# Performance work log

Hardware: AMD Instinct MI355X
Metric: run time of the kernel (lower is better)

The kernel has to match this reference:

```python
import jax, jax.numpy as jnp
import numpy as np

SEQ = 8192
IN_DIM = 1024
HIDDEN_DIM = 2048
N_EXPERTS = 8
TOPK = 2


def setup_inputs() -> dict:
    key = jax.random.key(0)
    ks = jax.random.split(key, 6)
    scale = 0.02
    inp = jax.random.normal(ks[0], (SEQ, IN_DIM), jnp.float32)
    weights = jax.random.uniform(ks[1], (SEQ, TOPK), jnp.float32)
    selections = jax.random.randint(ks[2], (SEQ, TOPK), 0, N_EXPERTS, jnp.int32)
    up_proj = jax.random.normal(ks[3], (HIDDEN_DIM * N_EXPERTS, IN_DIM), jnp.float32) * scale
    gate_proj = jax.random.normal(ks[4], (HIDDEN_DIM * N_EXPERTS, IN_DIM), jnp.float32) * scale
    down_proj = jax.random.normal(ks[5], (HIDDEN_DIM * N_EXPERTS, IN_DIM), jnp.float32) * scale
    return {"inp": inp, "weights": weights, "up_proj": up_proj,
            "gate_proj": gate_proj, "down_proj": down_proj, "selections": selections}


def reference(inp, weights, up_proj, gate_proj, down_proj, selections):
    seq, in_dim = inp.shape
    topk = selections.shape[-1]
    # dispatch: replicate each token topk times -> (seq*topk, in_dim)
    x = jnp.broadcast_to(inp[:, None, :], (seq, topk, in_dim)).reshape(-1, in_dim)
    e_ids = selections.reshape(-1)  # (seq*topk,) expert id per dispatched token
    W_up = up_proj.reshape(N_EXPERTS, HIDDEN_DIM, in_dim)
    W_gate = gate_proj.reshape(N_EXPERTS, HIDDEN_DIM, in_dim)
    W_down = down_proj.reshape(N_EXPERTS, HIDDEN_DIM, in_dim)
    out = jnp.zeros_like(x)
    # grouped (block-sparse) GEMM: loop over the small fixed expert set,
    # masking tokens not routed to this expert (gelu(0)*0 = 0, so math matches).
    for e in range(N_EXPERTS):
        mask = (e_ids == e)[:, None]
        xe = jnp.where(mask, x, 0.0)
        h = xe @ W_up[e].T        # (seq*topk, hidden)
        g = xe @ W_gate[e].T      # (seq*topk, hidden)
        out = out + jnp.where(mask, (jax.nn.gelu(g) * h) @ W_down[e], 0.0)
    # combine: weighted sum over topk expert outputs per token
    return (out.reshape(seq, topk, in_dim) * weights[:, :, None]).sum(axis=1)
```

## Files before the change

kernel.cpp:

```cpp
#include <hip/hip_runtime.h>


#define SEQ 8192
#define IN_DIM 1024
#define HID 2048
#define NEXP 8
#define TOPK 2
#define NSLOT (SEQ * TOPK)

#define BM 128
#define BK 64
#define BM1 256
#define MAX_T1 72

typedef unsigned short ushort_t;
typedef __bf16 bf16x8 __attribute__((ext_vector_type(8)));
typedef float f32x4 __attribute__((ext_vector_type(4)));

__device__ __forceinline__ ushort_t f2bf(float f) {
    union { float f; unsigned u; } v;
    v.f = f;
    unsigned r = v.u + 0x7FFFu + ((v.u >> 16) & 1u);
    return (ushort_t)(r >> 16);
}

__device__ __forceinline__ float gelu_tanh(float x) {
    float u = 0.7978845608028654f * x * (1.0f + 0.044715f * x * x);
    return x / (1.0f + __expf(-2.0f * u));
}

__device__ __forceinline__ void async16(const void* g, void* l) {
    __builtin_amdgcn_global_load_lds(
        (const __attribute__((address_space(1))) unsigned int*)g,
        (__attribute__((address_space(3))) unsigned int*)l, 16, 0, 0);
}

__global__ void cast_bf16_kernel(const float* __restrict__ in,
                                 ushort_t* __restrict__ out, int n) {
    int i = (blockIdx.x * blockDim.x + threadIdx.x) * 4;
    if (i >= n) return;
    float4 v = *(const float4*)(in + i);
    union { ushort_t u[4]; uint2 v; } o;
    o.u[0] = f2bf(v.x); o.u[1] = f2bf(v.y);
    o.u[2] = f2bf(v.z); o.u[3] = f2bf(v.w);
    *(uint2*)(out + i) = o.v;
}

__global__ void transpose_cast_kernel(const float* __restrict__ in,
                                      ushort_t* __restrict__ out) {
    __shared__ float tile[32][33];
    int e = blockIdx.z;
    int d0 = blockIdx.x * 32, h0 = blockIdx.y * 32;
    int tx = threadIdx.x & 31, ty = threadIdx.x >> 5;
    const float* src = in + (size_t)e * HID * IN_DIM;
    for (int j = 0; j < 32; j += 8)
        tile[ty + j][tx] = src[(size_t)(h0 + ty + j) * IN_DIM + d0 + tx];
    __syncthreads();
    ushort_t* dst = out + (size_t)e * IN_DIM * HID;
    for (int j = 0; j < 32; j += 8)
        dst[(size_t)(d0 + ty + j) * HID + h0 + tx] = f2bf(tile[tx][ty + j]);
}

__global__ void route_kernel(const int* __restrict__ sel,
                             const float* __restrict__ wts,
                             int* __restrict__ meta,
                             int* __restrict__ stok,
                             int* __restrict__ sinv) {
    __shared__ int lc[256][NEXP];
    __shared__ int tot[NEXP];
    __shared__ int s_off[NEXP + 1];
    int t = threadIdx.x;
    int cnt[NEXP];
#pragma unroll
    for (int e = 0; e < NEXP; e++) cnt[e] = 0;
    int base = t * (NSLOT / 256);
    for (int i = 0; i < NSLOT / 256; i++) cnt[sel[base + i]]++;
#pragma unroll
    for (int e = 0; e < NEXP; e++) lc[t][e] = cnt[e];
    __syncthreads();
    if (t < NEXP) {
        int run = 0;
        for (int i = 0; i < 256; i++) { int v = lc[i][t]; lc[i][t] = run; run += v; }
        tot[t] = run;
    }
    __syncthreads();
    if (t == 0) {
        int o = 0;
        for (int e = 0; e < NEXP; e++) { s_off[e] = o; o += tot[e]; }
        s_off[NEXP] = o;
        for (int e = 0; e <= NEXP; e++) meta[e] = s_off[e];
        int nt = 0;
        for (int e = 0; e < NEXP; e++) {
            int c = s_off[e + 1] - s_off[e];
            int m = (c + BM - 1) / BM;
            for (int i = 0; i < m; i++) { meta[32 + 2 * nt] = e; meta[33 + 2 * nt] = i; nt++; }
        }
        meta[16] = nt;
    }
    __syncthreads();
    int cur[NEXP];
#pragma unroll
    for (int e = 0; e < NEXP; e++) cur[e] = s_off[e] + lc[t][e];
    for (int i = 0; i < NSLOT / 256; i++) {
        int slot = base + i;
        int e = sel[slot];
        int pos = cur[e]++;
        stok[pos] = slot >> 1;
        sinv[slot] = pos;
    }
}

#define ST_A(b, h, koff) {                                                 \
        async16(pA[h][0] + (koff), &AT[b][h][(w * 16) * BK]);              \
        async16(pA[h][1] + (koff), &AT[b][h][(w * 16 + 8) * BK]); }
#define ST_U(b, koff) {                                                    \
        async16(pU[0] + (koff), &UT[b][(w * 16) * BK]);                    \
        async16(pU[1] + (koff), &UT[b][(w * 16 + 8) * BK]); }
#define ST_G(b, koff) {                                                    \
        async16(pG[0] + (koff), &GT[b][(w * 16) * BK]);                    \
        async16(pG[1] + (koff), &GT[b][(w * 16 + 8) * BK]); }

#define RD_A(b, mb) {                                                      \
        _Pragma("unroll") for (int mi = 0; mi < 4; mi++)                   \
        _Pragma("unroll") for (int kh = 0; kh < 2; kh++)                   \
            a[mi][kh] = *(const bf16x8*)&AT[b][wm][                        \
                ((mb) + mi * 16 + r4) * BK + (((kh * 4 + q) ^ sw7) << 3)]; }
#define RD_U(b) {                                                          \
        _Pragma("unroll") for (int ni = 0; ni < 2; ni++)                   \
        _Pragma("unroll") for (int kh = 0; kh < 2; kh++)                   \
            bu[ni][kh] = *(const bf16x8*)&UT[b][                           \
                (wn * 32 + ni * 16 + r4) * BK + (((kh * 4 + q) ^ sw7) << 3)]; }
#define RD_G(b) {                                                          \
        _Pragma("unroll") for (int ni = 0; ni < 2; ni++)                   \
        _Pragma("unroll") for (int kh = 0; kh < 2; kh++)                   \
            bg[ni][kh] = *(const bf16x8*)&GT[b][                           \
                (wn * 32 + ni * 16 + r4) * BK + (((kh * 4 + q) ^ sw7) << 3)]; }

#define MM(ACC, mb2, BB) {                                                 \
        _Pragma("unroll") for (int mi = 0; mi < 4; mi++)                   \
        _Pragma("unroll") for (int ni = 0; ni < 2; ni++)                   \
        _Pragma("unroll") for (int kh = 0; kh < 2; kh++)                   \
            ACC[(mb2) + mi][ni] = __builtin_amdgcn_mfma_f32_16x16x32_bf16( \
                a[mi][kh], BB[ni][kh], ACC[(mb2) + mi][ni], 0, 0, 0); }

#define BARRIER __builtin_amdgcn_s_barrier()
#define LGKM0 asm volatile("s_waitcnt lgkmcnt(0)" ::: "memory")
#define VMW2 asm volatile("s_waitcnt vmcnt(2)" ::: "memory")
#define VMW0 asm volatile("s_waitcnt vmcnt(0)" ::: "memory")
#define PRIO1 __builtin_amdgcn_s_setprio(1)
#define PRIO0 __builtin_amdgcn_s_setprio(0)

#define KPRO                                                               \
    ST_A(0, 0, 0); ST_A(0, 1, 0); ST_U(0, 0); ST_G(0, 0);                  \
    ST_A(1, 0, 64);                                                        \
    VMW2; BARRIER;

#define KBODY_FULL                                                         \
    RD_A(0, 0); RD_U(0); ST_A(1, 1, 64); BARRIER; LGKM0;                   \
    PRIO1; MM(accH, 0, bu); PRIO0; BARRIER;                                \
    RD_G(0); ST_U(1, 64); BARRIER; LGKM0;                                  \
    PRIO1; MM(accG, 0, bg); PRIO0; BARRIER;                                \
    RD_A(0, 64); ST_G(1, 64); BARRIER; LGKM0;                              \
    PRIO1; MM(accG, 4, bg); PRIO0; BARRIER;                                \
    ST_A(0, 0, 128); VMW2; BARRIER;                                        \
    PRIO1; MM(accH, 4, bu); PRIO0; BARRIER;                                \
    RD_A(1, 0); RD_U(1); ST_A(0, 1, 128); BARRIER; LGKM0;                  \
    PRIO1; MM(accH, 0, bu); PRIO0; BARRIER;                                \
    RD_G(1); ST_U(0, 128); BARRIER; LGKM0;                                 \
    PRIO1; MM(accG, 0, bg); PRIO0; BARRIER;                                \
    RD_A(1, 64); ST_G(0, 128); BARRIER; LGKM0;                             \
    PRIO1; MM(accG, 4, bg); PRIO0; BARRIER;                                \
    ST_A(1, 0, 192); VMW2; BARRIER;                                        \
    PRIO1; MM(accH, 4, bu); PRIO0; BARRIER;

#define KBODY_ADV {                                                        \
    pA[0][0] += 128; pA[0][1] += 128; pA[1][0] += 128; pA[1][1] += 128;    \
    pU[0] += 128; pU[1] += 128; pG[0] += 128; pG[1] += 128; }

#define KBODY_TAIL                                                         \
    RD_A(0, 0); RD_U(0); ST_A(1, 1, 64); BARRIER; LGKM0;                   \
    PRIO1; MM(accH, 0, bu); PRIO0; BARRIER;                                \
    RD_G(0); ST_U(1, 64); BARRIER; LGKM0;                                  \
    PRIO1; MM(accG, 0, bg); PRIO0; BARRIER;                                \
    RD_A(0, 64); ST_G(1, 64); BARRIER; LGKM0;                              \
    PRIO1; MM(accG, 4, bg); PRIO0; BARRIER;                                \
    VMW0; BARRIER;                                                         \
    PRIO1; MM(accH, 4, bu); PRIO0; BARRIER;                                \
    RD_A(1, 0); RD_U(1); BARRIER; LGKM0;                                   \
    PRIO1; MM(accH, 0, bu); PRIO0; BARRIER;                                \
    RD_G(1); BARRIER; LGKM0;                                               \
    PRIO1; MM(accG, 0, bg); PRIO0; BARRIER;                                \
    RD_A(1, 64); BARRIER; LGKM0;                                           \
    PRIO1; MM(accG, 4, bg); PRIO0; BARRIER;                                \
    PRIO1; MM(accH, 4, bu); PRIO0;

#define TILE_DERIVE(tile)                                                  \
    int e = -1, mt = 0, accT = 0;                                          \
    _Pragma("unroll")                                                      \
    for (int ee = 0; ee < NEXP; ee++) {                                    \
        int c = meta[ee + 1] - meta[ee];                                   \
        int m = (c + BM1 - 1) >> 8;                                        \
        if ((tile) >= accT && (tile) < accT + m) { e = ee; mt = (tile) - accT; } \
        accT += m;                                                         \
    }                                                                      \
    if (e < 0) return;                                                     \
    int off = meta[e];                                                     \
    int cnt = meta[e + 1] - off;                                           \
    int m0 = mt * BM1;

__global__ __launch_bounds__(512, 2) void gemm1_kernel(
    const ushort_t* __restrict__ X,
    const ushort_t* __restrict__ U,
    const ushort_t* __restrict__ G,
    const int* __restrict__ meta,
    const int* __restrict__ stok,
    ushort_t* __restrict__ act) {
    __shared__ __align__(16) ushort_t AT[2][2][128 * BK];
    __shared__ __align__(16) ushort_t UT[2][128 * BK];
    __shared__ __align__(16) ushort_t GT[2][128 * BK];
    __shared__ int s_tok[BM1];

    int id = blockIdx.x + MAX_T1 * blockIdx.y;
    int wi = (id & 7) * 144 + (id >> 3);
    int tile = wi % MAX_T1;
    int n0 = (wi / MAX_T1) * 128;

    TILE_DERIVE(tile);

    int tid = threadIdx.x;
    if (tid < BM1) {
        int r = m0 + tid;
        if (r >= cnt) r = cnt - 1;
        s_tok[tid] = stok[off + r];
    }
    __syncthreads();

    int lane = tid & 63;
    int w = tid >> 6;
    int wm = w >> 2;
    int wn = w & 3;
    int srow = lane >> 3;
    int schunk = lane & 7;
    int gchunk = schunk ^ srow;
    int r4 = lane & 15;
    int q = lane >> 4;
    int sw7 = r4 & 7;

    const ushort_t* pA[2][2];
#pragma unroll
    for (int h = 0; h < 2; h++)
#pragma unroll
        for (int j = 0; j < 2; j++) {
            int r = h * 128 + w * 16 + j * 8 + srow;
            pA[h][j] = X + (size_t)s_tok[r] * IN_DIM + gchunk * 8;
        }
    const ushort_t* Ue = U + ((size_t)e * HID + n0) * IN_DIM;
    const ushort_t* Ge = G + ((size_t)e * HID + n0) * IN_DIM;
    const ushort_t* pU[2];
    const ushort_t* pG[2];
#pragma unroll
    for (int j = 0; j < 2; j++) {
        int r = w * 16 + j * 8 + srow;
        pU[j] = Ue + (size_t)r * IN_DIM + gchunk * 8;
        pG[j] = Ge + (size_t)r * IN_DIM + gchunk * 8;
    }

    f32x4 accH[8][2], accG[8][2];
#pragma unroll
    for (int mi = 0; mi < 8; mi++)
#pragma unroll
        for (int ni = 0; ni < 2; ni++) {
            accH[mi][ni] = (f32x4){0.f, 0.f, 0.f, 0.f};
            accG[mi][ni] = (f32x4){0.f, 0.f, 0.f, 0.f};
        }

    bf16x8 a[4][2], bu[2][2], bg[2][2];

    KPRO;
#pragma unroll 1
    for (int i = 0; i < (IN_DIM / BK) / 2 - 1; ++i) {
        KBODY_FULL;
        KBODY_ADV;
    }
    KBODY_TAIL;

#pragma unroll
    for (int mf = 0; mf < 8; mf++) {
#pragma unroll
        for (int r = 0; r < 4; r++) {
            int row_local = wm * 128 + mf * 16 + q * 4 + r;
            int grow = m0 + row_local;
            if (grow >= cnt) continue;
            size_t orow = (size_t)(off + grow) * HID + n0 + wn * 32;
#pragma unroll
            for (int ni = 0; ni < 2; ni++) {
                float h = accH[mf][ni][r];
                float g = accG[mf][ni][r];
                act[orow + ni * 16 + r4] = f2bf(gelu_tanh(g) * h);
            }
        }
    }
}

__global__ __launch_bounds__(512, 2) void gemm2_kernel(
    const ushort_t* __restrict__ act,
    const ushort_t* __restrict__ DT,
    const int* __restrict__ meta,
    float* __restrict__ y) {
    __shared__ __align__(16) ushort_t AT[2][2][128 * BK];
    __shared__ __align__(16) ushort_t UT[2][128 * BK];
    __shared__ __align__(16) ushort_t GT[2][128 * BK];

    int id = blockIdx.x + MAX_T1 * blockIdx.y;
    int wi = (id & 7) * 36 + (id >> 3);
    int tile = wi % MAX_T1;
    int n0 = (wi / MAX_T1) * 256;

    TILE_DERIVE(tile);

    int tid = threadIdx.x;
    int lane = tid & 63;
    int w = tid >> 6;
    int wm = w >> 2;
    int wn = w & 3;
    int srow = lane >> 3;
    int schunk = lane & 7;
    int gchunk = schunk ^ srow;
    int r4 = lane & 15;
    int q = lane >> 4;
    int sw7 = r4 & 7;

    const ushort_t* Ae = act + (size_t)off * HID;
    const ushort_t* pA[2][2];
#pragma unroll
    for (int h = 0; h < 2; h++)
#pragma unroll
        for (int j = 0; j < 2; j++) {
            int ar = m0 + h * 128 + w * 16 + j * 8 + srow;
            if (ar >= cnt) ar = cnt - 1;
            pA[h][j] = Ae + (size_t)ar * HID + gchunk * 8;
        }
    const ushort_t* Be = DT + ((size_t)e * IN_DIM + n0) * HID;
    const ushort_t* pU[2];
    const ushort_t* pG[2];
#pragma unroll
    for (int j = 0; j < 2; j++) {
        int r = w * 16 + j * 8 + srow;
        pU[j] = Be + (size_t)r * HID + gchunk * 8;
        pG[j] = Be + (size_t)(128 + r) * HID + gchunk * 8;
    }

    f32x4 accH[8][2], accG[8][2];
#pragma unroll
    for (int mi = 0; mi < 8; mi++)
#pragma unroll
        for (int ni = 0; ni < 2; ni++) {
            accH[mi][ni] = (f32x4){0.f, 0.f, 0.f, 0.f};
            accG[mi][ni] = (f32x4){0.f, 0.f, 0.f, 0.f};
        }

    bf16x8 a[4][2], bu[2][2], bg[2][2];

    KPRO;
#pragma unroll 1
    for (int i = 0; i < (HID / BK) / 2 - 1; ++i) {
        KBODY_FULL;
        KBODY_ADV;
    }
    KBODY_TAIL;

#pragma unroll
    for (int mf = 0; mf < 8; mf++) {
#pragma unroll
        for (int r = 0; r < 4; r++) {
            int row_local = wm * 128 + mf * 16 + q * 4 + r;
            int grow = m0 + row_local;
            if (grow >= cnt) continue;
            float* orow = y + (size_t)(off + grow) * IN_DIM + n0 + wn * 32;
#pragma unroll
            for (int ni = 0; ni < 2; ni++) {
                orow[ni * 16 + r4] = accH[mf][ni][r];
                orow[128 + ni * 16 + r4] = accG[mf][ni][r];
            }
        }
    }
}

__global__ __launch_bounds__(256) void combine_kernel(
    const float* __restrict__ y,
    const float* __restrict__ wts,
    const int* __restrict__ sinv,
    float* __restrict__ out) {
    int tok = blockIdx.x;
    int c = threadIdx.x;
    int p0 = sinv[tok * 2], p1 = sinv[tok * 2 + 1];
    float w0 = wts[tok * 2], w1 = wts[tok * 2 + 1];
    float4 a = *(const float4*)(y + (size_t)p0 * IN_DIM + c * 4);
    float4 b = *(const float4*)(y + (size_t)p1 * IN_DIM + c * 4);
    float4 o;
    o.x = w0 * a.x + w1 * b.x;
    o.y = w0 * a.y + w1 * b.y;
    o.z = w0 * a.z + w1 * b.z;
    o.w = w0 * a.w + w1 * b.w;
    *(float4*)(out + (size_t)tok * IN_DIM + c * 4) = o;
}

extern "C" void kernel_launch(void* const* d_in, const int* in_sizes, int n_in,
                              void* d_out, int out_size, void* d_ws, size_t ws_size,
                              hipStream_t stream) {
    const float* inp  = (const float*)d_in[0];
    const float* wts  = (const float*)d_in[1];
    const float* up   = (const float*)d_in[2];
    const float* gate = (const float*)d_in[3];
    const float* down = (const float*)d_in[4];
    const int*   sel  = (const int*)d_in[5];
    float* out = (float*)d_out;

    char* ws = (char*)d_ws;
    ushort_t* inp_bf  = (ushort_t*)(ws);
    ushort_t* up_bf   = (ushort_t*)(ws + 16777216);
    ushort_t* gate_bf = (ushort_t*)(ws + 50331648);
    ushort_t* down_bf = (ushort_t*)(ws + 83886080);
    ushort_t* act     = (ushort_t*)(ws + 117440512);
    int*      stok    = (int*)(ws + 184549376);
    int*      sinv    = (int*)(ws + 184614912);
    int*      meta    = (int*)(ws + 184680448);
    float*    y       = (float*)(ws);

    cast_bf16_kernel<<<(SEQ * IN_DIM) / 1024, 256, 0, stream>>>(inp, inp_bf, SEQ * IN_DIM);
    cast_bf16_kernel<<<(NEXP * HID * IN_DIM) / 1024, 256, 0, stream>>>(up, up_bf, NEXP * HID * IN_DIM);
    cast_bf16_kernel<<<(NEXP * HID * IN_DIM) / 1024, 256, 0, stream>>>(gate, gate_bf, NEXP * HID * IN_DIM);
    transpose_cast_kernel<<<dim3(IN_DIM / 32, HID / 32, NEXP), 256, 0, stream>>>(down, down_bf);
    route_kernel<<<1, 256, 0, stream>>>(sel, wts, meta, stok, sinv);
    gemm1_kernel<<<dim3(MAX_T1, HID / 128), 512, 0, stream>>>(inp_bf, up_bf, gate_bf, meta, stok, act);
    gemm2_kernel<<<dim3(MAX_T1, IN_DIM / 256), 512, 0, stream>>>(act, down_bf, meta, y);
    combine_kernel<<<SEQ, 256, 0, stream>>>(y, wts, sinv, out);
}
```

Measured before the change: 567.1 us.

## Shrink gemm2 M-tile to 128 with new pipeline, fuse casts, remap XCD tiles

The down-projection GEMM now uses 128-row M tiles instead of 256, which roughly doubles the number of blocks (up to 140 tiles times 4 N-blocks) and reduces padding waste at the ragged end of each expert's token range. It gets a new double-buffered, single-k-step pipeline with finer vmcnt waits. The three input/up/gate fp32-to-bf16 cast launches are merged into one kernel. The gemm1 block-to-tile mapping is changed so that blocks on the same XCD share N-columns, aiming for better L2 reuse of weights. The trade-off is that smaller tiles lower per-block arithmetic intensity and reuse more weight traffic per output row.

```diff
diff --git a/kernel.cpp b/kernel.cpp
--- a/kernel.cpp
+++ b/kernel.cpp
@@ -12,6 +12,7 @@
 #define BK 64
 #define BM1 256
 #define MAX_T1 72
+#define MAX_T2 140
 
 typedef unsigned short ushort_t;
 typedef __bf16 bf16x8 __attribute__((ext_vector_type(8)));
@@ -35,15 +36,25 @@
         (__attribute__((address_space(3))) unsigned int*)l, 16, 0, 0);
 }
 
-__global__ void cast_bf16_kernel(const float* __restrict__ in,
-                                 ushort_t* __restrict__ out, int n) {
-    int i = (blockIdx.x * blockDim.x + threadIdx.x) * 4;
-    if (i >= n) return;
-    float4 v = *(const float4*)(in + i);
+__global__ void cast3_kernel(const float* __restrict__ inp,
+                             const float* __restrict__ up,
+                             const float* __restrict__ gate,
+                             ushort_t* __restrict__ o_inp,
+                             ushort_t* __restrict__ o_up,
+                             ushort_t* __restrict__ o_gate) {
+    const int N1 = SEQ * IN_DIM;
+    const int N2 = NEXP * HID * IN_DIM;
+    long i = (long)(blockIdx.x * blockDim.x + threadIdx.x) * 4;
+    const float* src;
+    ushort_t* dst;
+    if (i < N1)            { src = inp  + i;            dst = o_inp  + i; }
+    else if (i < N1 + N2)  { src = up   + (i - N1);     dst = o_up   + (i - N1); }
+    else                   { src = gate + (i - N1 - N2); dst = o_gate + (i - N1 - N2); }
+    float4 v = *(const float4*)src;
     union { ushort_t u[4]; uint2 v; } o;
     o.u[0] = f2bf(v.x); o.u[1] = f2bf(v.y);
     o.u[2] = f2bf(v.z); o.u[3] = f2bf(v.w);
-    *(uint2*)(out + i) = o.v;
+    *(uint2*)dst = o.v;
 }
 
 __global__ void transpose_cast_kernel(const float* __restrict__ in,
@@ -145,6 +156,7 @@
 
 #define BARRIER __builtin_amdgcn_s_barrier()
 #define LGKM0 asm volatile("s_waitcnt lgkmcnt(0)" ::: "memory")
+#define VMW4 asm volatile("s_waitcnt vmcnt(4)" ::: "memory")
 #define VMW2 asm volatile("s_waitcnt vmcnt(2)" ::: "memory")
 #define VMW0 asm volatile("s_waitcnt vmcnt(0)" ::: "memory")
 #define PRIO1 __builtin_amdgcn_s_setprio(1)
@@ -194,20 +206,6 @@
     PRIO1; MM(accG, 4, bg); PRIO0; BARRIER;                                \
     PRIO1; MM(accH, 4, bu); PRIO0;
 
-#define TILE_DERIVE(tile)                                                  \
-    int e = -1, mt = 0, accT = 0;                                          \
-    _Pragma("unroll")                                                      \
-    for (int ee = 0; ee < NEXP; ee++) {                                    \
-        int c = meta[ee + 1] - meta[ee];                                   \
-        int m = (c + BM1 - 1) >> 8;                                        \
-        if ((tile) >= accT && (tile) < accT + m) { e = ee; mt = (tile) - accT; } \
-        accT += m;                                                         \
-    }                                                                      \
-    if (e < 0) return;                                                     \
-    int off = meta[e];                                                     \
-    int cnt = meta[e + 1] - off;                                           \
-    int m0 = mt * BM1;
-
 __global__ __launch_bounds__(512, 2) void gemm1_kernel(
     const ushort_t* __restrict__ X,
     const ushort_t* __restrict__ U,
@@ -221,11 +219,23 @@
     __shared__ int s_tok[BM1];
 
     int id = blockIdx.x + MAX_T1 * blockIdx.y;
-    int wi = (id & 7) * 144 + (id >> 3);
-    int tile = wi % MAX_T1;
-    int n0 = (wi / MAX_T1) * 128;
-
-    TILE_DERIVE(tile);
+    int xcd = id & 7;
+    int j = id >> 3;
+    int tile = j >> 1;
+    int n0 = ((xcd << 1) | (j & 1)) * 128;
+
+    int e = -1, mt = 0, accT = 0;
+#pragma unroll
+    for (int ee = 0; ee < NEXP; ee++) {
+        int c = meta[ee + 1] - meta[ee];
+        int m = (c + BM1 - 1) >> 8;
+        if (tile >= accT && tile < accT + m) { e = ee; mt = tile - accT; }
+        accT += m;
+    }
+    if (e < 0) return;
+    int off = meta[e];
+    int cnt = meta[e + 1] - off;
+    int m0 = mt * BM1;
 
     int tid = threadIdx.x;
     if (tid < BM1) {
@@ -250,19 +260,19 @@
 #pragma unroll
     for (int h = 0; h < 2; h++)
 #pragma unroll
-        for (int j = 0; j < 2; j++) {
-            int r = h * 128 + w * 16 + j * 8 + srow;
-            pA[h][j] = X + (size_t)s_tok[r] * IN_DIM + gchunk * 8;
+        for (int jj = 0; jj < 2; jj++) {
+            int r = h * 128 + w * 16 + jj * 8 + srow;
+            pA[h][jj] = X + (size_t)s_tok[r] * IN_DIM + gchunk * 8;
         }
     const ushort_t* Ue = U + ((size_t)e * HID + n0) * IN_DIM;
     const ushort_t* Ge = G + ((size_t)e * HID + n0) * IN_DIM;
     const ushort_t* pU[2];
     const ushort_t* pG[2];
 #pragma unroll
-    for (int j = 0; j < 2; j++) {
-        int r = w * 16 + j * 8 + srow;
-        pU[j] = Ue + (size_t)r * IN_DIM + gchunk * 8;
-        pG[j] = Ge + (size_t)r * IN_DIM + gchunk * 8;
+    for (int jj = 0; jj < 2; jj++) {
+        int r = w * 16 + jj * 8 + srow;
+        pU[jj] = Ue + (size_t)r * IN_DIM + gchunk * 8;
+        pG[jj] = Ge + (size_t)r * IN_DIM + gchunk * 8;
     }
 
     f32x4 accH[8][2], accG[8][2];
@@ -307,16 +317,29 @@
     const ushort_t* __restrict__ DT,
     const int* __restrict__ meta,
     float* __restrict__ y) {
-    __shared__ __align__(16) ushort_t AT[2][2][128 * BK];
-    __shared__ __align__(16) ushort_t UT[2][128 * BK];
-    __shared__ __align__(16) ushort_t GT[2][128 * BK];
-
-    int id = blockIdx.x + MAX_T1 * blockIdx.y;
-    int wi = (id & 7) * 36 + (id >> 3);
-    int tile = wi % MAX_T1;
-    int n0 = (wi / MAX_T1) * 256;
-
-    TILE_DERIVE(tile);
+    __shared__ __align__(16) ushort_t AT2[2][128 * BK];
+    __shared__ __align__(16) ushort_t UT2[2][128 * BK];
+    __shared__ __align__(16) ushort_t GT2[2][128 * BK];
+
+    int id = blockIdx.x + MAX_T2 * blockIdx.y;
+    int xcd = id & 7;
+    int jj0 = id >> 3;
+    int wk = xcd * 70 + jj0;
+    int tile = wk >> 2;
+    int n0 = (wk & 3) * 256;
+
+    int e = -1, mt = 0, accT = 0;
+#pragma unroll
+    for (int ee = 0; ee < NEXP; ee++) {
+        int c = meta[ee + 1] - meta[ee];
+        int m = (c + 127) >> 7;
+        if (tile >= accT && tile < accT + m) { e = ee; mt = tile - accT; }
+        accT += m;
+    }
+    if (e < 0) return;
+    int off = meta[e];
+    int cnt = meta[e + 1] - off;
+    int m0 = mt * 128;
 
     int tid = threadIdx.x;
     int lane = tid & 63;
@@ -331,56 +354,98 @@
     int sw7 = r4 & 7;
 
     const ushort_t* Ae = act + (size_t)off * HID;
-    const ushort_t* pA[2][2];
-#pragma unroll
-    for (int h = 0; h < 2; h++)
-#pragma unroll
-        for (int j = 0; j < 2; j++) {
-            int ar = m0 + h * 128 + w * 16 + j * 8 + srow;
-            if (ar >= cnt) ar = cnt - 1;
-            pA[h][j] = Ae + (size_t)ar * HID + gchunk * 8;
+    const ushort_t* pA2[2];
+#pragma unroll
+    for (int jj = 0; jj < 2; jj++) {
+        int ar = m0 + w * 16 + jj * 8 + srow;
+        if (ar >= cnt) ar = cnt - 1;
+        pA2[jj] = Ae + (size_t)ar * HID + gchunk * 8;
+    }
+    const ushort_t* Be = DT + ((size_t)e * IN_DIM + n0) * HID;
+    const ushort_t* pU2[2];
+    const ushort_t* pG2[2];
+#pragma unroll
+    for (int jj = 0; jj < 2; jj++) {
+        int r = w * 16 + jj * 8 + srow;
+        pU2[jj] = Be + (size_t)r * HID + gchunk * 8;
+        pG2[jj] = Be + (size_t)(128 + r) * HID + gchunk * 8;
+    }
+
+    f32x4 accU[4][2], accGG[4][2];
+#pragma unroll
+    for (int mi = 0; mi < 4; mi++)
+#pragma unroll
+        for (int ni = 0; ni < 2; ni++) {
+            accU[mi][ni] = (f32x4){0.f, 0.f, 0.f, 0.f};
+            accGG[mi][ni] = (f32x4){0.f, 0.f, 0.f, 0.f};
         }
-    const ushort_t* Be = DT + ((size_t)e * IN_DIM + n0) * HID;
-    const ushort_t* pU[2];
-    const ushort_t* pG[2];
-#pragma unroll
-    for (int j = 0; j < 2; j++) {
-        int r = w * 16 + j * 8 + srow;
-        pU[j] = Be + (size_t)r * HID + gchunk * 8;
-        pG[j] = Be + (size_t)(128 + r) * HID + gchunk * 8;
-    }
-
-    f32x4 accH[8][2], accG[8][2];
-#pragma unroll
-    for (int mi = 0; mi < 8; mi++)
-#pragma unroll
-        for (int ni = 0; ni < 2; ni++) {
-            accH[mi][ni] = (f32x4){0.f, 0.f, 0.f, 0.f};
-            accG[mi][ni] = (f32x4){0.f, 0.f, 0.f, 0.f};
-        }
 
     bf16x8 a[4][2], bu[2][2], bg[2][2];
 
-    KPRO;
+#define ST_A2(b, koff) {                                                   \
+        async16(pA2[0] + (koff), &AT2[b][(w * 16) * BK]);                  \
+        async16(pA2[1] + (koff), &AT2[b][(w * 16 + 8) * BK]); }
+#define ST_U2(b, koff) {                                                   \
+        async16(pU2[0] + (koff), &UT2[b][(w * 16) * BK]);                  \
+        async16(pU2[1] + (koff), &UT2[b][(w * 16 + 8) * BK]); }
+#define ST_G2(b, koff) {                                                   \
+        async16(pG2[0] + (koff), &GT2[b][(w * 16) * BK]);                  \
+        async16(pG2[1] + (koff), &GT2[b][(w * 16 + 8) * BK]); }
+#define RD_A2(b) {                                                         \
+        _Pragma("unroll") for (int mi = 0; mi < 4; mi++)                   \
+        _Pragma("unroll") for (int kh = 0; kh < 2; kh++)                   \
+            a[mi][kh] = *(const bf16x8*)&AT2[b][                           \
+                (wm * 64 + mi * 16 + r4) * BK + (((kh * 4 + q) ^ sw7) << 3)]; }
+#define RD_U2(b) {                                                         \
+        _Pragma("unroll") for (int ni = 0; ni < 2; ni++)                   \
+        _Pragma("unroll") for (int kh = 0; kh < 2; kh++)                   \
+            bu[ni][kh] = *(const bf16x8*)&UT2[b][                          \
+                (wn * 32 + ni * 16 + r4) * BK + (((kh * 4 + q) ^ sw7) << 3)]; }
+#define RD_G2(b) {                                                         \
+        _Pragma("unroll") for (int ni = 0; ni < 2; ni++)                   \
+        _Pragma("unroll") for (int kh = 0; kh < 2; kh++)                   \
+            bg[ni][kh] = *(const bf16x8*)&GT2[b][                          \
+                (wn * 32 + ni * 16 + r4) * BK + (((kh * 4 + q) ^ sw7) << 3)]; }
+
+#define G2BODY(b)                                                          \
+    RD_A2(b); RD_U2(b); ST_A2(b ^ 1, 64); ST_U2(b ^ 1, 64); BARRIER; LGKM0;\
+    PRIO1; MM(accU, 0, bu); PRIO0; VMW4; BARRIER;                          \
+    RD_G2(b); ST_G2(b ^ 1, 64); BARRIER; LGKM0;                            \
+    PRIO1; MM(accGG, 0, bg); PRIO0; VMW2; BARRIER;
+
+#define G2TAIL(b)                                                          \
+    RD_A2(b); RD_U2(b); BARRIER; LGKM0;                                    \
+    PRIO1; MM(accU, 0, bu); PRIO0; VMW0; BARRIER;                          \
+    RD_G2(b); BARRIER; LGKM0;                                              \
+    PRIO1; MM(accGG, 0, bg); PRIO0;
+
+#define G2ADV {                                                            \
+    pA2[0] += 64; pA2[1] += 64; pU2[0] += 64; pU2[1] += 64;                \
+    pG2[0] += 64; pG2[1] += 64; }
+
+    ST_A2(0, 0); ST_U2(0, 0); ST_G2(0, 0);
+    VMW2; BARRIER;
+
 #pragma unroll 1
-    for (int i = 0; i < (HID / BK) / 2 - 1; ++i) {
-        KBODY_FULL;
-        KBODY_ADV;
-    }
-    KBODY_TAIL;
-
-#pragma unroll
-    for (int mf = 0; mf < 8; mf++) {
+    for (int i = 0; i < 15; i++) {
+        G2BODY(0); G2ADV;
+        G2BODY(1); G2ADV;
+    }
+    G2BODY(0); G2ADV;
+    G2TAIL(1);
+
+#pragma unroll
+    for (int mi = 0; mi < 4; mi++) {
 #pragma unroll
         for (int r = 0; r < 4; r++) {
-            int row_local = wm * 128 + mf * 16 + q * 4 + r;
+            int row_local = wm * 64 + mi * 16 + q * 4 + r;
             int grow = m0 + row_local;
             if (grow >= cnt) continue;
             float* orow = y + (size_t)(off + grow) * IN_DIM + n0 + wn * 32;
 #pragma unroll
             for (int ni = 0; ni < 2; ni++) {
-                orow[ni * 16 + r4] = accH[mf][ni][r];
-                orow[128 + ni * 16 + r4] = accG[mf][ni][r];
+                orow[ni * 16 + r4] = accU[mi][ni][r];
+                orow[128 + ni * 16 + r4] = accGG[mi][ni][r];
             }
         }
     }
@@ -427,12 +492,12 @@
     int*      meta    = (int*)(ws + 184680448);
     float*    y       = (float*)(ws);
 
-    cast_bf16_kernel<<<(SEQ * IN_DIM) / 1024, 256, 0, stream>>>(inp, inp_bf, SEQ * IN_DIM);
-    cast_bf16_kernel<<<(NEXP * HID * IN_DIM) / 1024, 256, 0, stream>>>(up, up_bf, NEXP * HID * IN_DIM);
-    cast_bf16_kernel<<<(NEXP * HID * IN_DIM) / 1024, 256, 0, stream>>>(gate, gate_bf, NEXP * HID * IN_DIM);
+    const int CAST_N = SEQ * IN_DIM + 2 * NEXP * HID * IN_DIM;
+    cast3_kernel<<<CAST_N / 1024, 256, 0, stream>>>(inp, up, gate,
+                                                    inp_bf, up_bf, gate_bf);
     transpose_cast_kernel<<<dim3(IN_DIM / 32, HID / 32, NEXP), 256, 0, stream>>>(down, down_bf);
     route_kernel<<<1, 256, 0, stream>>>(sel, wts, meta, stok, sinv);
     gemm1_kernel<<<dim3(MAX_T1, HID / 128), 512, 0, stream>>>(inp_bf, up_bf, gate_bf, meta, stok, act);
-    gemm2_kernel<<<dim3(MAX_T1, IN_DIM / 256), 512, 0, stream>>>(act, down_bf, meta, y);
+    gemm2_kernel<<<dim3(MAX_T2, 4), 512, 0, stream>>>(act, down_bf, meta, y);
     combine_kernel<<<SEQ, 256, 0, stream>>>(y, wts, sinv, out);
 }
```

Result: no change. 572.9 us (+1.0%).
